# Optimization experiments

Measured on AMD Instinct MI355X. Metric: run time of the kernel, lower is better.

## Reference

```python
import jax, jax.numpy as jnp
import numpy as np

B, N, K, OUT = 8, 2048, 30, 13


def _knn_idx(x, k):
    # x: [B,N,F] -> indices of k nearest neighbors (squared L2, includes self)
    sq = jnp.sum(x * x, axis=-1)  # [B,N]
    d = sq[:, :, None] + sq[:, None, :] - 2.0 * jnp.einsum('bnf,bmf->bnm', x, x)
    _, idx = jax.lax.top_k(-d, k)  # [B,N,k]
    return idx


def _edge_conv(x, W1, b1, g, be, W2, b2, k):
    # DynamicEdgeConv: kNN on feature space, message = MLP([x_i, x_j - x_i]), max aggr
    idx = _knn_idx(x, k)                                  # [B,N,k] (non-differentiable)
    xj = jax.vmap(lambda xb, ib: xb[ib])(x, idx)          # gather neighbors [B,N,k,F]
    xi = x[:, :, None, :]
    e = jnp.concatenate([jnp.broadcast_to(xi, xj.shape), xj - xi], axis=-1)  # [B,N,k,2F]
    # PyG MLP([2F,64,64]): Linear + BN(eval: affine) + ReLU, then plain Linear
    h = jax.nn.relu((e @ W1 + b1) * g + be)
    h = h @ W2 + b2
    return jnp.max(h, axis=2)                             # max over k neighbors -> [B,N,64]


def setup_inputs():
    key = jax.random.key(0)
    ks = jax.random.split(key, 40)

    def lin(i, fin, fout):
        W = jax.random.normal(ks[i], (fin, fout), jnp.float32) / np.sqrt(fin)
        return W, jnp.zeros((fout,), jnp.float32)

    inp = {}
    inp['x'] = jax.random.normal(ks[0], (B, N, 3), jnp.float32)
    inp['pos'] = jax.random.normal(ks[1], (B, N, 3), jnp.float32)
    inp['batch'] = jnp.repeat(jnp.arange(B, dtype=jnp.int32), N)
    i = 2
    for name, fin in [('c1', 12), ('c2', 128), ('c3', 128)]:
        W1, b1 = lin(i, fin, 64); i += 1
        W2, b2 = lin(i, 64, 64); i += 1
        inp[name + '_W1'] = W1; inp[name + '_b1'] = b1
        inp[name + '_g'] = 1.0 + 0.1 * jax.random.normal(ks[i], (64,), jnp.float32); i += 1
        inp[name + '_be'] = 0.1 * jax.random.normal(ks[i], (64,), jnp.float32); i += 1
        inp[name + '_W2'] = W2; inp[name + '_b2'] = b2
    dims = [192, 1024, 256, 128, OUT]
    for j in range(4):
        W, b = lin(i, dims[j], dims[j + 1]); i += 1
        inp[f'm_W{j + 1}'] = W; inp[f'm_b{j + 1}'] = b
    return inp


def reference(x, pos, batch,
              c1_W1, c1_b1, c1_g, c1_be, c1_W2, c1_b2,
              c2_W1, c2_b1, c2_g, c2_be, c2_W2, c2_b2,
              c3_W1, c3_b1, c3_g, c3_be, c3_W2, c3_b2,
              m_W1, m_b1, m_W2, m_b2, m_W3, m_b3, m_W4, m_b4):
    x0 = jnp.concatenate([pos, x], axis=-1)               # [B,N,6]
    x1 = _edge_conv(x0, c1_W1, c1_b1, c1_g, c1_be, c1_W2, c1_b2, K)
    x2 = _edge_conv(x1, c2_W1, c2_b1, c2_g, c2_be, c2_W2, c2_b2, K)
    x3 = _edge_conv(x2, c3_W1, c3_b1, c3_g, c3_be, c3_W2, c3_b2, K)
    h = jnp.concatenate([x1, x2, x3], axis=-1)            # [B,N,192]
    # classifier MLP([192,1024,256,128,OUT], norm=None): Linear+ReLU(+dropout=eval id), plain last
    h = jax.nn.relu(h @ m_W1 + m_b1)
    h = jax.nn.relu(h @ m_W2 + m_b2)
    h = jax.nn.relu(h @ m_W3 + m_b3)
    out = h @ m_W4 + m_b4
    return jax.nn.log_softmax(out, axis=-1), x3
```

## Files before the change

kernel.cpp:

```cpp
#include <hip/hip_runtime.h>

using u32 = unsigned int;
typedef short s8v __attribute__((ext_vector_type(8)));
typedef short s4v __attribute__((ext_vector_type(4)));
typedef float f4v __attribute__((ext_vector_type(4)));

#define DEV static __device__ __forceinline__

DEV void cvt_split(float f, unsigned short& h, unsigned short& l) {
  u32 x = __builtin_bit_cast(u32, f);
  u32 rh = (x + 0x7FFFu + ((x >> 16) & 1u)) & 0xFFFF0000u;
  h = (unsigned short)(rh >> 16);
  float fl = f - __builtin_bit_cast(float, rh);
  u32 y = __builtin_bit_cast(u32, fl);
  l = (unsigned short)((y + 0x7FFFu + ((y >> 16) & 1u)) >> 16);
}

__global__ void k_build_x0(const float* __restrict__ x, const float* __restrict__ pos,
                           float* __restrict__ x0) {
  int p = blockIdx.x * 256 + threadIdx.x;
  float* o = x0 + (size_t)p * 8;
  o[0] = pos[p*3+0]; o[1] = pos[p*3+1]; o[2] = pos[p*3+2];
  o[3] = x[p*3+0];   o[4] = x[p*3+1];   o[5] = x[p*3+2];
  o[6] = 0.f; o[7] = 0.f;
}

__global__ void k_sqnorm(const float* __restrict__ x, int stride, int F,
                         float* __restrict__ sq) {
  int wid  = (blockIdx.x * 256 + threadIdx.x) >> 6;
  int lane = threadIdx.x & 63;
  float v = (lane < F) ? x[(size_t)wid * stride + lane] : 0.f;
  float s = v * v;
  #pragma unroll
  for (int m = 32; m; m >>= 1) s += __shfl_xor(s, m);
  if (lane == 0) sq[wid] = s;
}

template<int F>
__global__ __launch_bounds__(256) void k_dist(const float* __restrict__ x, int stride,
    const float* __restrict__ sq, int cbase, float* __restrict__ D) {
  constexpr int PAD = F + 4;
  __shared__ __align__(16) float Xi[128 * PAD];
  __shared__ __align__(16) float Xj[128 * PAD];
  __shared__ float SQI[128], SQJ[128];
  int b  = blockIdx.z;
  int i0 = cbase + blockIdx.y * 128;
  int j0 = blockIdx.x * 128;
  int tid = threadIdx.x;
  constexpr int NPASS = 128 * (F / 4) / 256;
  #pragma unroll
  for (int ps = 0; ps < NPASS; ++ps) {
    int e4 = ps * 256 + tid;
    int r = e4 / (F / 4), f4 = (e4 % (F / 4)) * 4;
    *(float4*)&Xi[r*PAD + f4] = *(const float4*)&x[(size_t)(b*2048 + i0 + r)*stride + f4];
    *(float4*)&Xj[r*PAD + f4] = *(const float4*)&x[(size_t)(b*2048 + j0 + r)*stride + f4];
  }
  if (tid < 128) {
    SQI[tid] = sq[b*2048 + i0 + tid];
    SQJ[tid] = sq[b*2048 + j0 + tid];
  }
  __syncthreads();
  int tx = tid & 15, ty = tid >> 4;
  float acc[8][8];
  #pragma unroll
  for (int i = 0; i < 8; ++i)
    #pragma unroll
    for (int j = 0; j < 8; ++j) acc[i][j] = 0.f;
  #pragma unroll 2
  for (int kf = 0; kf < F; kf += 4) {
    float4 av[8], wv[8];
    #pragma unroll
    for (int i = 0; i < 8; ++i) av[i] = *(const float4*)&Xi[(ty + 16*i)*PAD + kf];
    #pragma unroll
    for (int j = 0; j < 8; ++j) wv[j] = *(const float4*)&Xj[(tx + 16*j)*PAD + kf];
    #pragma unroll
    for (int i = 0; i < 8; ++i)
      #pragma unroll
      for (int j = 0; j < 8; ++j) {
        acc[i][j] += av[i].x * wv[j].x;
        acc[i][j] += av[i].y * wv[j].y;
        acc[i][j] += av[i].z * wv[j].z;
        acc[i][j] += av[i].w * wv[j].w;
      }
  }
  #pragma unroll
  for (int i = 0; i < 8; ++i) {
    int row = ty + 16*i;
    float si = SQI[row];
    #pragma unroll
    for (int j = 0; j < 8; ++j) {
      int col = tx + 16*j;
      D[(size_t)(b*512 + blockIdx.y*128 + row)*2048 + j0 + col] =
          si + SQJ[col] - 2.f * acc[i][j];
    }
  }
}

__global__ __launch_bounds__(256) void k_topk(const float* __restrict__ D, int cbase,
                                              int* __restrict__ knn) {
  int wid  = blockIdx.x * 4 + (threadIdx.x >> 6);
  int lane = threadIdx.x & 63;
  int b = wid >> 9, il = wid & 511;
  const float* row = D + (size_t)(b*512 + il) * 2048;
  float v[32];
  #pragma unroll
  for (int s = 0; s < 32; ++s) v[s] = row[lane + 64*s];
  const float INFV = __builtin_bit_cast(float, 0x7f800000u);
  int wj = 0;
  #pragma unroll 1
  for (int it = 0; it < 30; ++it) {
    float mv = v[0]; int ms = 0;
    #pragma unroll
    for (int s = 1; s < 32; ++s) {
      bool lt = v[s] < mv;
      mv = lt ? v[s] : mv;
      ms = lt ? s : ms;
    }
    int mj = lane + (ms << 6);
    #pragma unroll
    for (int m = 1; m < 64; m <<= 1) {
      float ov = __shfl_xor(mv, m);
      int   oj = __shfl_xor(mj, m);
      bool take = (ov < mv) || ((ov == mv) && (oj < mj));
      mv = take ? ov : mv;
      mj = take ? oj : mj;
    }
    int gj = __builtin_amdgcn_readfirstlane(mj);
    if (lane == it) wj = gj;
    int owner = gj & 63, slot = gj >> 6;
    #pragma unroll
    for (int s = 0; s < 32; ++s) {
      if (slot == s) {
        if (lane == owner) v[s] = INFV;
      }
    }
  }
  if (lane < 30) knn[(size_t)(b*2048 + cbase + il)*30 + lane] = b*2048 + wj;
}

__global__ __launch_bounds__(256) void k_prep(const float* __restrict__ x, int stride, int F,
    const float* __restrict__ W1, const float* __restrict__ b1,
    float* __restrict__ A0, float* __restrict__ V) {
  int p = blockIdx.x * 4 + (threadIdx.x >> 6);
  int lane = threadIdx.x & 63;
  float u = 0.f, v = 0.f;
  for (int f = 0; f < F; ++f) {
    float xv = x[(size_t)p*stride + f];
    float wa = W1[f*64 + lane];
    float wb = W1[(F + f)*64 + lane];
    u += xv * (wa - wb);
    v += xv * wb;
  }
  A0[p*64 + lane] = u + b1[lane];
  V[p*64 + lane]  = v;
}

__global__ __launch_bounds__(256) void k_edge(const float* __restrict__ A0,
    const float* __restrict__ V, const int* __restrict__ knn,
    const float* __restrict__ W2, const float* __restrict__ b2,
    const float* __restrict__ g, const float* __restrict__ be,
    float* __restrict__ out, int ostride) {
  int p = blockIdx.x * 4 + (threadIdx.x >> 6);
  int lane = threadIdx.x & 63;
  float w2c[64];
  #pragma unroll
  for (int c = 0; c < 64; ++c) w2c[c] = W2[c*64 + lane];
  float arow = A0[p*64 + lane];
  float gg = g[lane], bbe = be[lane];
  const int* kr = knn + p*30;
  float m = -3.0e38f;
  int j = kr[0];
  float vg = V[(size_t)j*64 + lane];
  #pragma unroll 1
  for (int k = 0; k < 30; ++k) {
    int jn = kr[k < 29 ? k + 1 : 29];
    float vgn = V[(size_t)jn*64 + lane];
    float pre = (arow + vg) * gg + bbe;
    float h1 = pre > 0.f ? pre : 0.f;
    u32 hb = __builtin_bit_cast(u32, h1);
    float s0 = 0.f, s1 = 0.f, s2 = 0.f, s3 = 0.f;
    #pragma unroll
    for (int c = 0; c < 64; c += 4) {
      s0 += __builtin_bit_cast(float, (u32)__builtin_amdgcn_readlane((int)hb, c+0)) * w2c[c+0];
      s1 += __builtin_bit_cast(float, (u32)__builtin_amdgcn_readlane((int)hb, c+1)) * w2c[c+1];
      s2 += __builtin_bit_cast(float, (u32)__builtin_amdgcn_readlane((int)hb, c+2)) * w2c[c+2];
      s3 += __builtin_bit_cast(float, (u32)__builtin_amdgcn_readlane((int)hb, c+3)) * w2c[c+3];
    }
    float h2 = (s0 + s1) + (s2 + s3);
    m = m > h2 ? m : h2;
    vg = vgn;
  }
  out[(size_t)p*ostride + lane] = m + b2[lane];
}

__global__ __launch_bounds__(256) void k_mlp(const float* __restrict__ Ag, int lda,
    const float* __restrict__ Wg, const float* __restrict__ bg,
    float* __restrict__ Cg, int ldc, int N, int K, int dorelu) {
  constexpr int PK = 40;
  __shared__ __align__(16) unsigned short Ah[128*PK];
  __shared__ __align__(16) unsigned short Al[128*PK];
  __shared__ __align__(16) unsigned short Wh[128*PK];
  __shared__ __align__(16) unsigned short Wl[128*PK];
  int tid  = threadIdx.x;
  int wave = tid >> 6, lane = tid & 63;
  int wm = (wave >> 1) * 64, wn = (wave & 1) * 64;
  int lr = lane & 15, kb = lane >> 4;
  int m0 = blockIdx.y * 128, n0 = blockIdx.x * 128;

  f4v acc[4][4];
  #pragma unroll
  for (int i = 0; i < 4; ++i)
    #pragma unroll
    for (int j = 0; j < 4; ++j) acc[i][j] = (f4v)(0.f);

  for (int k0 = 0; k0 < K; k0 += 32) {
    #pragma unroll
    for (int p = 0; p < 4; ++p) {
      int e4 = p * 256 + tid;
      int r = e4 >> 3, c4 = (e4 & 7) << 2;
      float4 a = *(const float4*)&Ag[(size_t)(m0 + r)*lda + k0 + c4];
      unsigned short h0,h1,h2,h3,l0,l1,l2,l3;
      cvt_split(a.x, h0, l0); cvt_split(a.y, h1, l1);
      cvt_split(a.z, h2, l2); cvt_split(a.w, h3, l3);
      *(s4v*)&Ah[r*PK + c4] = s4v{(short)h0,(short)h1,(short)h2,(short)h3};
      *(s4v*)&Al[r*PK + c4] = s4v{(short)l0,(short)l1,(short)l2,(short)l3};
    }
    #pragma unroll
    for (int p = 0; p < 4; ++p) {
      int e4 = p * 256 + tid;
      int kr = e4 >> 5, nc4 = (e4 & 31) << 2;
      float4 w = *(const float4*)&Wg[(size_t)(k0 + kr)*N + n0 + nc4];
      unsigned short h, l;
      cvt_split(w.x, h, l); Wh[(nc4+0)*PK + kr] = h; Wl[(nc4+0)*PK + kr] = l;
      cvt_split(w.y, h, l); Wh[(nc4+1)*PK + kr] = h; Wl[(nc4+1)*PK + kr] = l;
      cvt_split(w.z, h, l); Wh[(nc4+2)*PK + kr] = h; Wl[(nc4+2)*PK + kr] = l;
      cvt_split(w.w, h, l); Wh[(nc4+3)*PK + kr] = h; Wl[(nc4+3)*PK + kr] = l;
    }
    __syncthreads();

    s8v bh[4], bl[4];
    #pragma unroll
    for (int jf = 0; jf < 4; ++jf) {
      int n = wn + jf*16 + lr;
      bh[jf] = *(const s8v*)&Wh[n*PK + kb*8];
      bl[jf] = *(const s8v*)&Wl[n*PK + kb*8];
    }
    #pragma unroll
    for (int mf = 0; mf < 4; ++mf) {
      int m = wm + mf*16 + lr;
      s8v ah = *(const s8v*)&Ah[m*PK + kb*8];
      s8v al = *(const s8v*)&Al[m*PK + kb*8];
      #pragma unroll
      for (int jf = 0; jf < 4; ++jf) {
        acc[mf][jf] = __builtin_amdgcn_mfma_f32_16x16x32_bf16(ah, bh[jf], acc[mf][jf], 0, 0, 0);
        acc[mf][jf] = __builtin_amdgcn_mfma_f32_16x16x32_bf16(ah, bl[jf], acc[mf][jf], 0, 0, 0);
        acc[mf][jf] = __builtin_amdgcn_mfma_f32_16x16x32_bf16(al, bh[jf], acc[mf][jf], 0, 0, 0);
      }
    }
    __syncthreads();
  }

  #pragma unroll
  for (int jf = 0; jf < 4; ++jf) {
    int n = n0 + wn + jf*16 + lr;
    float bb = bg[n];
    #pragma unroll
    for (int mf = 0; mf < 4; ++mf) {
      #pragma unroll
      for (int r = 0; r < 4; ++r) {
        int m = m0 + wm + mf*16 + kb*4 + r;
        float v = acc[mf][jf][r] + bb;
        if (dorelu) v = v > 0.f ? v : 0.f;
        Cg[(size_t)m*ldc + n] = v;
      }
    }
  }
}

__global__ __launch_bounds__(256) void k_head(const float* __restrict__ H3,
    const float* __restrict__ W4, const float* __restrict__ b4,
    float* __restrict__ out0, int pbase) {
  __shared__ float w4s[128 * 13];
  __shared__ float b4s[13];
  for (int e = threadIdx.x; e < 128*13; e += 256) w4s[e] = W4[e];
  if (threadIdx.x < 13) b4s[threadIdx.x] = b4[threadIdx.x];
  __syncthreads();
  int pl = blockIdx.x * 256 + threadIdx.x;
  float acc[13];
  #pragma unroll
  for (int c = 0; c < 13; ++c) acc[c] = b4s[c];
  const float* hr = H3 + (size_t)pl * 128;
  #pragma unroll 1
  for (int k = 0; k < 128; k += 4) {
    float4 h = *(const float4*)&hr[k];
    #pragma unroll
    for (int c = 0; c < 13; ++c) {
      acc[c] += h.x * w4s[(k+0)*13 + c];
      acc[c] += h.y * w4s[(k+1)*13 + c];
      acc[c] += h.z * w4s[(k+2)*13 + c];
      acc[c] += h.w * w4s[(k+3)*13 + c];
    }
  }
  float mx = acc[0];
  #pragma unroll
  for (int c = 1; c < 13; ++c) mx = fmaxf(mx, acc[c]);
  float s = 0.f;
  #pragma unroll
  for (int c = 0; c < 13; ++c) s += expf(acc[c] - mx);
  float lg = logf(s);
  size_t ob = (size_t)(pbase + pl) * 13;
  #pragma unroll
  for (int c = 0; c < 13; ++c) out0[ob + c] = acc[c] - mx - lg;
}

__global__ void k_out1(const float* __restrict__ hcat, float* __restrict__ out1) {
  int e = blockIdx.x * 256 + threadIdx.x;
  int p = e >> 6, c = e & 63;
  out1[e] = hcat[(size_t)p*192 + 128 + c];
}

extern "C" void kernel_launch(void* const* d_in, const int* in_sizes, int n_in,
                              void* d_out, int out_size, void* d_ws, size_t ws_size,
                              hipStream_t stream) {
  (void)in_sizes; (void)n_in; (void)out_size; (void)ws_size;
  const float* x   = (const float*)d_in[0];
  const float* pos = (const float*)d_in[1];
  const float* cw[3][6];
  for (int c = 0; c < 3; ++c)
    for (int t = 0; t < 6; ++t)
      cw[c][t] = (const float*)d_in[3 + c*6 + t];
  const float *mW[4], *mb[4];
  for (int j = 0; j < 4; ++j) {
    mW[j] = (const float*)d_in[21 + 2*j];
    mb[j] = (const float*)d_in[22 + 2*j];
  }

  float* ws   = (float*)d_ws;
  float* x0   = ws;
  float* sq   = x0 + 131072;
  int*   knn  = (int*)(sq + 16384);
  float* A0   = (float*)(knn + 491520);
  float* V    = A0 + 1048576;
  float* hcat = V + 1048576;
  float* U    = hcat + 3145728;
  float* H2c  = U + 8388608;
  float* H3c  = H2c + 2097152;

  float* out0 = (float*)d_out;
  float* out1 = out0 + 8*2048*13;

  k_build_x0<<<64, 256, 0, stream>>>(x, pos, x0);

  for (int c = 0; c < 3; ++c) {
    const float* xin; int stride, F, Fsq;
    if (c == 0)      { xin = x0;        stride = 8;   F = 6;  Fsq = 8;  }
    else if (c == 1) { xin = hcat;      stride = 192; F = 64; Fsq = 64; }
    else             { xin = hcat + 64; stride = 192; F = 64; Fsq = 64; }
    k_sqnorm<<<4096, 256, 0, stream>>>(xin, stride, Fsq, sq);
    for (int ch = 0; ch < 4; ++ch) {
      if (c == 0) k_dist<8> <<<dim3(16,4,8), 256, 0, stream>>>(xin, stride, sq, ch*512, U);
      else        k_dist<64><<<dim3(16,4,8), 256, 0, stream>>>(xin, stride, sq, ch*512, U);
      k_topk<<<1024, 256, 0, stream>>>(U, ch*512, knn);
    }
    k_prep<<<4096, 256, 0, stream>>>(xin, stride, F, cw[c][0], cw[c][1], A0, V);
    k_edge<<<4096, 256, 0, stream>>>(A0, V, knn, cw[c][4], cw[c][5], cw[c][2], cw[c][3],
                                     hcat + 64*c, 192);
  }

  for (int ch = 0; ch < 2; ++ch) {
    const float* Ain = hcat + (size_t)ch * 8192 * 192;
    k_mlp<<<dim3(8,64), 256, 0, stream>>>(Ain, 192,  mW[0], mb[0], U,   1024, 1024, 192,  1);
    k_mlp<<<dim3(2,64), 256, 0, stream>>>(U,   1024, mW[1], mb[1], H2c, 256,  256,  1024, 1);
    k_mlp<<<dim3(1,64), 256, 0, stream>>>(H2c, 256,  mW[2], mb[2], H3c, 128,  128,  256,  1);
    k_head<<<32, 256, 0, stream>>>(H3c, mW[3], mb[3], out0, ch*8192);
  }
  k_out1<<<4096, 256, 0, stream>>>(hcat, out1);
}
```

Before: 1.588 ms.

## Pre-split MLP weights to bf16 hi/lo and use MFMA for third edge conv

Adds a kernel that converts weight matrices once into transposed bf16 high/low pairs, so the MLP GEMMs load B fragments straight from global memory instead of converting and staging weights in shared memory each k-step. The MLP kernel is templated on N-fragments per wave, giving the 256- and 128-wide layers smaller tiles and more blocks. The third edge conv gets a new MFMA-based kernel that builds the 30x64 hidden activations per point as split-bf16 fragments and does the max-reduction with shuffles. It adds extra conversion launches and reuses workspace regions, and the 3-pass split-bf16 scheme may lose a little precision against fp32.

Result: faster. 1.343 ms (-15.4%).

```diff
diff --git a/kernel.cpp b/kernel.cpp
--- a/kernel.cpp
+++ b/kernel.cpp
@@ -1,5 +1,6 @@
 #include <hip/hip_runtime.h>
 
+using u16 = unsigned short;
 using u32 = unsigned int;
 typedef short s8v __attribute__((ext_vector_type(8)));
 typedef short s4v __attribute__((ext_vector_type(4)));
@@ -7,13 +8,24 @@
 
 #define DEV static __device__ __forceinline__
 
-DEV void cvt_split(float f, unsigned short& h, unsigned short& l) {
+DEV void cvt_split(float f, u16& h, u16& l) {
   u32 x = __builtin_bit_cast(u32, f);
   u32 rh = (x + 0x7FFFu + ((x >> 16) & 1u)) & 0xFFFF0000u;
-  h = (unsigned short)(rh >> 16);
+  h = (u16)(rh >> 16);
   float fl = f - __builtin_bit_cast(float, rh);
   u32 y = __builtin_bit_cast(u32, fl);
-  l = (unsigned short)((y + 0x7FFFu + ((y >> 16) & 1u)) >> 16);
+  l = (u16)((y + 0x7FFFu + ((y >> 16) & 1u)) >> 16);
+}
+
+__global__ void k_splitw(const float* __restrict__ W, int K, int N, int PK,
+                         u16* __restrict__ Wh, u16* __restrict__ Wl) {
+  int e = blockIdx.x * 256 + threadIdx.x;
+  if (e >= K * N) return;
+  int k = e / N, n = e % N;
+  u16 h, l;
+  cvt_split(W[e], h, l);
+  Wh[(size_t)n * PK + k] = h;
+  Wl[(size_t)n * PK + k] = l;
 }
 
 __global__ void k_build_x0(const float* __restrict__ x, const float* __restrict__ pos,
@@ -155,7 +167,7 @@
   V[p*64 + lane]  = v;
 }
 
-__global__ __launch_bounds__(256) void k_edge(const float* __restrict__ A0,
+__global__ __launch_bounds__(256) void k_edge_v(const float* __restrict__ A0,
     const float* __restrict__ V, const int* __restrict__ knn,
     const float* __restrict__ W2, const float* __restrict__ b2,
     const float* __restrict__ g, const float* __restrict__ be,
@@ -193,65 +205,151 @@
   out[(size_t)p*ostride + lane] = m + b2[lane];
 }
 
+__global__ __launch_bounds__(256) void k_edge_m(const float* __restrict__ A0,
+    const float* __restrict__ V, const int* __restrict__ knn,
+    const u16* __restrict__ W2h, const u16* __restrict__ W2l,
+    const float* __restrict__ b2,
+    const float* __restrict__ g, const float* __restrict__ be,
+    float* __restrict__ out, int ostride) {
+  constexpr int PKW = 72;
+  int p = blockIdx.x * 4 + (threadIdx.x >> 6);
+  int lane = threadIdx.x & 63;
+  int lr = lane & 15, kb = lane >> 4;
+
+  const int* kr = knn + (size_t)p * 30;
+  int j0 = kr[lr];
+  int j1 = kr[lr + 16 < 30 ? lr + 16 : 29];
+
+  s8v bh[4][2], bl[4][2];
+  #pragma unroll
+  for (int jf = 0; jf < 4; ++jf) {
+    int n = jf*16 + lr;
+    #pragma unroll
+    for (int ks = 0; ks < 2; ++ks) {
+      bh[jf][ks] = *(const s8v*)&W2h[n*PKW + ks*32 + kb*8];
+      bl[jf][ks] = *(const s8v*)&W2l[n*PKW + ks*32 + kb*8];
+    }
+  }
+
+  float base[2][8], gs[2][8];
+  #pragma unroll
+  for (int ks = 0; ks < 2; ++ks) {
+    int cb = ks*32 + kb*8;
+    float4 a0 = *(const float4*)&A0[(size_t)p*64 + cb];
+    float4 a1 = *(const float4*)&A0[(size_t)p*64 + cb + 4];
+    float4 g0 = *(const float4*)&g[cb];
+    float4 g1 = *(const float4*)&g[cb + 4];
+    float4 e0 = *(const float4*)&be[cb];
+    float4 e1 = *(const float4*)&be[cb + 4];
+    base[ks][0]=a0.x*g0.x+e0.x; base[ks][1]=a0.y*g0.y+e0.y;
+    base[ks][2]=a0.z*g0.z+e0.z; base[ks][3]=a0.w*g0.w+e0.w;
+    base[ks][4]=a1.x*g1.x+e1.x; base[ks][5]=a1.y*g1.y+e1.y;
+    base[ks][6]=a1.z*g1.z+e1.z; base[ks][7]=a1.w*g1.w+e1.w;
+    gs[ks][0]=g0.x; gs[ks][1]=g0.y; gs[ks][2]=g0.z; gs[ks][3]=g0.w;
+    gs[ks][4]=g1.x; gs[ks][5]=g1.y; gs[ks][6]=g1.z; gs[ks][7]=g1.w;
+  }
+
+  s8v ah[2][2], al[2][2];
+  #pragma unroll
+  for (int mt = 0; mt < 2; ++mt) {
+    const float* vr = V + (size_t)(mt ? j1 : j0) * 64;
+    #pragma unroll
+    for (int ks = 0; ks < 2; ++ks) {
+      int cb = ks*32 + kb*8;
+      float4 v0 = *(const float4*)&vr[cb];
+      float4 v1 = *(const float4*)&vr[cb + 4];
+      float hv[8];
+      hv[0]=base[ks][0]+v0.x*gs[ks][0]; hv[1]=base[ks][1]+v0.y*gs[ks][1];
+      hv[2]=base[ks][2]+v0.z*gs[ks][2]; hv[3]=base[ks][3]+v0.w*gs[ks][3];
+      hv[4]=base[ks][4]+v1.x*gs[ks][4]; hv[5]=base[ks][5]+v1.y*gs[ks][5];
+      hv[6]=base[ks][6]+v1.z*gs[ks][6]; hv[7]=base[ks][7]+v1.w*gs[ks][7];
+      s8v hfrag, lfrag;
+      #pragma unroll
+      for (int e = 0; e < 8; ++e) {
+        float h1 = hv[e] > 0.f ? hv[e] : 0.f;
+        u16 hh, ll;
+        cvt_split(h1, hh, ll);
+        hfrag[e] = (short)hh; lfrag[e] = (short)ll;
+      }
+      ah[mt][ks] = hfrag; al[mt][ks] = lfrag;
+    }
+  }
+
+  f4v acc[2][4];
+  #pragma unroll
+  for (int mt = 0; mt < 2; ++mt)
+    #pragma unroll
+    for (int jf = 0; jf < 4; ++jf) acc[mt][jf] = (f4v)(0.f);
+
+  #pragma unroll
+  for (int mt = 0; mt < 2; ++mt)
+    #pragma unroll
+    for (int jf = 0; jf < 4; ++jf)
+      #pragma unroll
+      for (int ks = 0; ks < 2; ++ks) {
+        acc[mt][jf] = __builtin_amdgcn_mfma_f32_16x16x32_bf16(ah[mt][ks], bh[jf][ks], acc[mt][jf], 0, 0, 0);
+        acc[mt][jf] = __builtin_amdgcn_mfma_f32_16x16x32_bf16(ah[mt][ks], bl[jf][ks], acc[mt][jf], 0, 0, 0);
+        acc[mt][jf] = __builtin_amdgcn_mfma_f32_16x16x32_bf16(al[mt][ks], bh[jf][ks], acc[mt][jf], 0, 0, 0);
+      }
+
+  #pragma unroll
+  for (int jf = 0; jf < 4; ++jf) {
+    float m = fmaxf(fmaxf(acc[0][jf][0], acc[0][jf][1]), fmaxf(acc[0][jf][2], acc[0][jf][3]));
+    float m1 = fmaxf(fmaxf(acc[1][jf][0], acc[1][jf][1]), fmaxf(acc[1][jf][2], acc[1][jf][3]));
+    m = fmaxf(m, m1);
+    m = fmaxf(m, __shfl_xor(m, 16));
+    m = fmaxf(m, __shfl_xor(m, 32));
+    if (kb == 0) out[(size_t)p*ostride + jf*16 + lr] = m + b2[jf*16 + lr];
+  }
+}
+
+template<int NJF>
 __global__ __launch_bounds__(256) void k_mlp(const float* __restrict__ Ag, int lda,
-    const float* __restrict__ Wg, const float* __restrict__ bg,
+    const u16* __restrict__ Wth, const u16* __restrict__ Wtl, int PKW,
+    const float* __restrict__ bg,
     float* __restrict__ Cg, int ldc, int N, int K, int dorelu) {
   constexpr int PK = 40;
-  __shared__ __align__(16) unsigned short Ah[128*PK];
-  __shared__ __align__(16) unsigned short Al[128*PK];
-  __shared__ __align__(16) unsigned short Wh[128*PK];
-  __shared__ __align__(16) unsigned short Wl[128*PK];
+  __shared__ __align__(16) u16 Ah[128*PK];
+  __shared__ __align__(16) u16 Al[128*PK];
   int tid  = threadIdx.x;
   int wave = tid >> 6, lane = tid & 63;
-  int wm = (wave >> 1) * 64, wn = (wave & 1) * 64;
+  int wm = (wave >> 1) * 64, wn = (wave & 1) * (NJF*16);
   int lr = lane & 15, kb = lane >> 4;
-  int m0 = blockIdx.y * 128, n0 = blockIdx.x * 128;
-
-  f4v acc[4][4];
+  int m0 = blockIdx.y * 128, n0 = blockIdx.x * (2*NJF*16);
+
+  f4v acc[4][NJF];
   #pragma unroll
   for (int i = 0; i < 4; ++i)
     #pragma unroll
-    for (int j = 0; j < 4; ++j) acc[i][j] = (f4v)(0.f);
+    for (int j = 0; j < NJF; ++j) acc[i][j] = (f4v)(0.f);
 
   for (int k0 = 0; k0 < K; k0 += 32) {
-    #pragma unroll
-    for (int p = 0; p < 4; ++p) {
-      int e4 = p * 256 + tid;
+    s8v bh[NJF], bl[NJF];
+    #pragma unroll
+    for (int jf = 0; jf < NJF; ++jf) {
+      int n = n0 + wn + jf*16 + lr;
+      bh[jf] = *(const s8v*)&Wth[(size_t)n*PKW + k0 + kb*8];
+      bl[jf] = *(const s8v*)&Wtl[(size_t)n*PKW + k0 + kb*8];
+    }
+    #pragma unroll
+    for (int ps = 0; ps < 4; ++ps) {
+      int e4 = ps * 256 + tid;
       int r = e4 >> 3, c4 = (e4 & 7) << 2;
       float4 a = *(const float4*)&Ag[(size_t)(m0 + r)*lda + k0 + c4];
-      unsigned short h0,h1,h2,h3,l0,l1,l2,l3;
+      u16 h0,h1,h2,h3,l0,l1,l2,l3;
       cvt_split(a.x, h0, l0); cvt_split(a.y, h1, l1);
       cvt_split(a.z, h2, l2); cvt_split(a.w, h3, l3);
       *(s4v*)&Ah[r*PK + c4] = s4v{(short)h0,(short)h1,(short)h2,(short)h3};
       *(s4v*)&Al[r*PK + c4] = s4v{(short)l0,(short)l1,(short)l2,(short)l3};
     }
-    #pragma unroll
-    for (int p = 0; p < 4; ++p) {
-      int e4 = p * 256 + tid;
-      int kr = e4 >> 5, nc4 = (e4 & 31) << 2;
-      float4 w = *(const float4*)&Wg[(size_t)(k0 + kr)*N + n0 + nc4];
-      unsigned short h, l;
-      cvt_split(w.x, h, l); Wh[(nc4+0)*PK + kr] = h; Wl[(nc4+0)*PK + kr] = l;
-      cvt_split(w.y, h, l); Wh[(nc4+1)*PK + kr] = h; Wl[(nc4+1)*PK + kr] = l;
-      cvt_split(w.z, h, l); Wh[(nc4+2)*PK + kr] = h; Wl[(nc4+2)*PK + kr] = l;
-      cvt_split(w.w, h, l); Wh[(nc4+3)*PK + kr] = h; Wl[(nc4+3)*PK + kr] = l;
-    }
     __syncthreads();
-
-    s8v bh[4], bl[4];
-    #pragma unroll
-    for (int jf = 0; jf < 4; ++jf) {
-      int n = wn + jf*16 + lr;
-      bh[jf] = *(const s8v*)&Wh[n*PK + kb*8];
-      bl[jf] = *(const s8v*)&Wl[n*PK + kb*8];
-    }
     #pragma unroll
     for (int mf = 0; mf < 4; ++mf) {
       int m = wm + mf*16 + lr;
       s8v ah = *(const s8v*)&Ah[m*PK + kb*8];
       s8v al = *(const s8v*)&Al[m*PK + kb*8];
       #pragma unroll
-      for (int jf = 0; jf < 4; ++jf) {
+      for (int jf = 0; jf < NJF; ++jf) {
         acc[mf][jf] = __builtin_amdgcn_mfma_f32_16x16x32_bf16(ah, bh[jf], acc[mf][jf], 0, 0, 0);
         acc[mf][jf] = __builtin_amdgcn_mfma_f32_16x16x32_bf16(ah, bl[jf], acc[mf][jf], 0, 0, 0);
         acc[mf][jf] = __builtin_amdgcn_mfma_f32_16x16x32_bf16(al, bh[jf], acc[mf][jf], 0, 0, 0);
@@ -261,7 +359,7 @@
   }
 
   #pragma unroll
-  for (int jf = 0; jf < 4; ++jf) {
+  for (int jf = 0; jf < NJF; ++jf) {
     int n = n0 + wn + jf*16 + lr;
     float bb = bg[n];
     #pragma unroll
@@ -345,11 +443,17 @@
   float* U    = hcat + 3145728;
   float* H2c  = U + 8388608;
   float* H3c  = H2c + 2097152;
+  u16* eW2 = (u16*)(H3c + 1048576);
+  u16* mwp = (u16*)A0;
+  u16* m1h = mwp;            u16* m1l = m1h + 204800;
+  u16* m2h = m1l + 204800;   u16* m2l = m2h + 264192;
+  u16* m3h = m2l + 264192;   u16* m3l = m3h + 33792;
 
   float* out0 = (float*)d_out;
   float* out1 = out0 + 8*2048*13;
 
   k_build_x0<<<64, 256, 0, stream>>>(x, pos, x0);
+  k_splitw<<<16, 256, 0, stream>>>(cw[2][4], 64, 64, 72, eW2, eW2 + 4608);
 
   for (int c = 0; c < 3; ++c) {
     const float* xin; int stride, F, Fsq;
@@ -363,15 +467,23 @@
       k_topk<<<1024, 256, 0, stream>>>(U, ch*512, knn);
     }
     k_prep<<<4096, 256, 0, stream>>>(xin, stride, F, cw[c][0], cw[c][1], A0, V);
-    k_edge<<<4096, 256, 0, stream>>>(A0, V, knn, cw[c][4], cw[c][5], cw[c][2], cw[c][3],
-                                     hcat + 64*c, 192);
-  }
+    if (c < 2)
+      k_edge_v<<<4096, 256, 0, stream>>>(A0, V, knn, cw[c][4], cw[c][5],
+                                         cw[c][2], cw[c][3], hcat + 64*c, 192);
+    else
+      k_edge_m<<<4096, 256, 0, stream>>>(A0, V, knn, eW2, eW2 + 4608,
+                                         cw[c][5], cw[c][2], cw[c][3], hcat + 64*c, 192);
+  }
+
+  k_splitw<<<768,  256, 0, stream>>>(mW[0], 192,  1024, 200,  m1h, m1l);
+  k_splitw<<<1024, 256, 0, stream>>>(mW[1], 1024, 256,  1032, m2h, m2l);
+  k_splitw<<<128,  256, 0, stream>>>(mW[2], 256,  128,  264,  m3h, m3l);
 
   for (int ch = 0; ch < 2; ++ch) {
     const float* Ain = hcat + (size_t)ch * 8192 * 192;
-    k_mlp<<<dim3(8,64), 256, 0, stream>>>(Ain, 192,  mW[0], mb[0], U,   1024, 1024, 192,  1);
-    k_mlp<<<dim3(2,64), 256, 0, stream>>>(U,   1024, mW[1], mb[1], H2c, 256,  256,  1024, 1);
-    k_mlp<<<dim3(1,64), 256, 0, stream>>>(H2c, 256,  mW[2], mb[2], H3c, 128,  128,  256,  1);
+    k_mlp<4><<<dim3(8,64), 256, 0, stream>>>(Ain, 192,  m1h, m1l, 200,  mb[0], U,   1024, 1024, 192,  1);
+    k_mlp<2><<<dim3(4,64), 256, 0, stream>>>(U,   1024, m2h, m2l, 1032, mb[1], H2c, 256,  256,  1024, 1);
+    k_mlp<2><<<dim3(2,64), 256, 0, stream>>>(H2c, 256,  m3h, m3l, 264,  mb[2], H3c, 128,  128,  256,  1);
     k_head<<<32, 256, 0, stream>>>(H3c, mW[3], mb[3], out0, ch*8192);
   }
   k_out1<<<4096, 256, 0, stream>>>(hcat, out1);
```
